# Kernel optimization log

Hardware: AMD Instinct MI355X
Metric: run time of the kernel (lower is better)

Reference implementation:

```python
import jax, jax.numpy as jnp
import numpy as np

N_NODES = 10000
N_EDGES = 100000
D_IN = 2 * 1280   # concat of row/col node embeddings
H1 = 512
H2 = 256


def gcn_conv(x, edge_index, W, b):
    """PyG GCNConv: add self-loops, symmetric deg^-1/2 normalization,
    x @ W then scatter-add of normalized messages, plus bias.
    num_nodes is inferred from x.shape[0] (here = n_edges, faithful to source)."""
    N = x.shape[0]
    loops = jnp.arange(N, dtype=edge_index.dtype)
    row = jnp.concatenate([edge_index[0], loops])  # sources
    col = jnp.concatenate([edge_index[1], loops])  # targets
    deg = jax.ops.segment_sum(jnp.ones_like(row, dtype=x.dtype), col, num_segments=N)
    dinv = jax.lax.rsqrt(deg)  # deg >= 1 thanks to self-loops
    norm = dinv[row] * dinv[col]  # [E+N]
    h = x @ W  # [N, out]
    out = jax.ops.segment_sum(h[row] * norm[:, None], col, num_segments=N)
    return out + b


def setup_inputs() -> dict:
    key = jax.random.key(0)
    ks = jax.random.split(key, 9)
    x = jax.random.normal(ks[0], (N_NODES, 1280), dtype=jnp.float32)
    edge_index = jax.random.randint(ks[1], (2, N_EDGES), 0, N_NODES, dtype=jnp.int32)
    # uniform noise for gumbel-sigmoid (torch.rand); keep strictly in (0,1)
    eps = jax.random.uniform(ks[2], (N_EDGES, 1), jnp.float32, 1e-6, 1.0 - 1e-6)
    W1 = jax.random.normal(ks[3], (D_IN, H1), jnp.float32) * (1.0 / np.sqrt(D_IN))
    b1 = jnp.zeros((H1,), jnp.float32)
    W2 = jax.random.normal(ks[4], (H1, H2), jnp.float32) * (1.0 / np.sqrt(H1))
    b2 = jnp.zeros((H2,), jnp.float32)
    Wl = jax.random.normal(ks[5], (H2, 1), jnp.float32) * (1.0 / np.sqrt(H2))
    bl = jnp.zeros((1,), jnp.float32)
    return {"x": x, "edge_index": edge_index, "eps": eps,
            "W1": W1, "b1": b1, "W2": W2, "b2": b2, "Wl": Wl, "bl": bl}


def reference(x, edge_index, eps, W1, b1, W2, b2, Wl, bl):
    rows, cols = edge_index[0], edge_index[1]
    # per-edge explainer input: concat of endpoint embeddings -> [E, 2560]
    input_embs = jnp.concatenate([x[rows], x[cols]], axis=1)
    h = jax.nn.relu(gcn_conv(input_embs, edge_index, W1, b1))
    h = jax.nn.relu(gcn_conv(h, edge_index, W2, b2))
    pre = h @ Wl + bl  # [E, 1] sampling weights
    # gumbel-sigmoid sampling (temperature = 1.0)
    gate = jnp.log(eps) - jnp.log1p(-eps) + pre
    mask = jax.nn.sigmoid(gate)
    pos, neg = mask, 1.0 - mask
    kld = jnp.mean(pos * jnp.log(pos / 0.5 + 1e-8) + neg * jnp.log(neg / 0.5 + 1e-9))
    return (kld, mask)
```

## Files before the change

kernel.cpp:

```cpp
#include <hip/hip_runtime.h>
#include <cstdint>
#include <cstddef>

#define H1DIM 512
#define H2DIM 256
#define DNODE 1280
#define NPACK 1024

typedef __attribute__((ext_vector_type(8))) short short8v;
typedef __attribute__((ext_vector_type(4))) float f32x4;
typedef __attribute__((ext_vector_type(4))) unsigned short us4;

__device__ __forceinline__ unsigned short f2bf(float f) {
    unsigned int u = __builtin_bit_cast(unsigned int, f);
    u += 0x7fffu + ((u >> 16) & 1u);
    return (unsigned short)(u >> 16);
}
__device__ __forceinline__ float bf2f(unsigned short h) {
    unsigned int u = ((unsigned int)h) << 16;
    return __builtin_bit_cast(float, u);
}

__device__ __forceinline__ int cmi(int R, int kq) {
    return ((R >> 4) << 9) + (((kq >> 3) << 4) + (R & 15)) * 8;
}

__global__ __launch_bounds__(1024) void scan_dinv_k(
    const int* __restrict__ hist, int* __restrict__ off, int* __restrict__ cursor,
    float* __restrict__ dinv, int N)
{
    __shared__ int part[1024];
    const int t = threadIdx.x;
    const int per = (N + 1023) / 1024;
    const int base = t * per;
    int s = 0;
    for (int i = 0; i < per; ++i) { int b = base + i; if (b < N) s += hist[b]; }
    part[t] = s;
    __syncthreads();
    for (int d = 1; d < 1024; d <<= 1) {
        int v = (t >= d) ? part[t - d] : 0;
        __syncthreads();
        part[t] += v;
        __syncthreads();
    }
    int run = (t == 0) ? 0 : part[t - 1];
    for (int i = 0; i < per; ++i) {
        int b = base + i;
        if (b < N) {
            int h = hist[b];
            off[b] = run;
            run += h;
            cursor[b] = 0;
            dinv[b] = rsqrtf(1.0f + (float)h);
        }
    }
    if (t == 1023) off[N] = run;
}
__global__ void fill_k(const int* __restrict__ e0, const int* __restrict__ e1,
                       const int* __restrict__ off, int* __restrict__ cursor,
                       int* __restrict__ srcs, int E) {
    int e = blockIdx.x * 256 + threadIdx.x;
    if (e < E) {
        int t = e1[e];
        int p = off[t] + atomicAdd(&cursor[t], 1);
        srcs[p] = e0[e];
    }
}

__global__ __launch_bounds__(256) void prep_k(
    const float* __restrict__ x, unsigned short* __restrict__ xb, int ncvt, int ntot,
    const int* __restrict__ e1, int* __restrict__ hist, int nhist, int E,
    const float* __restrict__ W1, unsigned short* __restrict__ Bpt1,
    const float* __restrict__ W2, unsigned short* __restrict__ W2t)
{
    __shared__ float tile[32][33];
    int b = blockIdx.x;

    if (b < ncvt) {
        int i = b * 256 + threadIdx.x;
        if (i * 4 < ntot) {
            f32x4 v = *reinterpret_cast<const f32x4*>(x + (size_t)i * 4);
            us4 o;
            o[0] = f2bf(v.x); o[1] = f2bf(v.y); o[2] = f2bf(v.z); o[3] = f2bf(v.w);
            *reinterpret_cast<us4*>(xb + (size_t)i * 4) = o;
        }
        return;
    }
    b -= ncvt;
    if (b < nhist) {
        int e = b * 256 + threadIdx.x;
        if (e < E) atomicAdd(&hist[e1[e]], 1);
        return;
    }
    b -= nhist;

    const float* src; unsigned short* dst; int ldsrc, lddst, bx, by;
    if (b < 640) {
        src = W1; dst = Bpt1; ldsrc = H1DIM; lddst = DNODE; bx = b & 15; by = b >> 4;
    } else if (b < 1280) {
        b -= 640;
        src = W1 + (size_t)DNODE * H1DIM; dst = Bpt1 + (size_t)H1DIM * DNODE;
        ldsrc = H1DIM; lddst = DNODE; bx = b & 15; by = b >> 4;
    } else {
        b -= 1280;
        src = W2; dst = W2t; ldsrc = H2DIM; lddst = H1DIM; bx = b & 7; by = b >> 3;
    }
    const int c0 = bx * 32, r0 = by * 32;
    const int tx = threadIdx.x & 31;
    const int ty = threadIdx.x >> 5;
#pragma unroll
    for (int rr = ty; rr < 32; rr += 8)
        tile[rr][tx] = src[(size_t)(r0 + rr) * ldsrc + c0 + tx];
    __syncthreads();
#pragma unroll
    for (int rr = ty; rr < 32; rr += 8)
        dst[(size_t)(c0 + rr) * lddst + r0 + tx] = f2bf(tile[tx][rr]);
}

template <int MODE>
__global__ __launch_bounds__(512) void gemm_u_k(
    const unsigned short* __restrict__ Ab,
    const unsigned short* __restrict__ Bt,
    unsigned short* __restrict__ Cb,
    const unsigned short* __restrict__ out1b,
    const unsigned short* __restrict__ XWb16,
    const float* __restrict__ b1,
    const float* __restrict__ b2,
    const float* __restrict__ Wl,
    const int* __restrict__ e0, const int* __restrict__ e1,
    unsigned short* __restrict__ h2b, float* __restrict__ pre_raw,
    int M, int K, int Nn, int nwg)
{
    __shared__ alignas(16) unsigned short As[2][128 * 32];
    __shared__ alignas(16) unsigned short Bs[2][256 * 32];
    __shared__ float b1s[H1DIM];
    __shared__ float b2s[H2DIM];
    __shared__ float wls[H2DIM];
    __shared__ float preacc[128];

    const int tid  = threadIdx.x;
    const int lane = tid & 63;
    const int w    = tid >> 6;
    const int wm   = w >> 2, wn = w & 3;

    int mb, n0;
    if (MODE == 0) {
        const int q = nwg >> 3, r = nwg & 7;
        const int xcd = blockIdx.x & 7;
        const int base = (xcd < r) ? xcd * (q + 1) : r * (q + 1) + (xcd - r) * q;
        const int wg = base + (blockIdx.x >> 3);
        mb = wg >> 2;
        n0 = (wg & 3) << 8;
    } else {
        mb = blockIdx.x;
        n0 = 0;
    }
    const int m0 = mb * 128;

    if (MODE == 1) {
        if (tid < 128) preacc[tid] = 0.f;
        if (tid < 256) { b2s[tid] = b2[tid]; wls[tid] = Wl[tid]; }
        b1s[tid] = b1[tid];
    }

    const int sa_r = tid >> 2, sa_k = (tid & 3) << 3;
    const int sb_r = tid >> 1, sb_k = (tid & 1) << 4;
    const int gma  = m0 + sa_r;
    const bool aval = (gma < M);

    const int aw  = cmi(sa_r, sa_k);
    const int bw0 = cmi(sb_r, sb_k);
    const int bw1 = cmi(sb_r, sb_k + 8);

    const unsigned short* bsrc = Bt + (size_t)(n0 + sb_r) * K + sb_k;
    const unsigned short* s1 = nullptr;
    const unsigned short* s2 = nullptr;
    bool dual = false;
    if (MODE == 0) {
        if (aval) s1 = Ab + (size_t)gma * K + sa_k;
    } else if (aval) {
        if (gma < Nn) {
            s1 = out1b + (size_t)gma * H1DIM + sa_k;
        } else {
            s1 = XWb16 + (size_t)e0[gma] * NPACK + sa_k;
            s2 = XWb16 + (size_t)e1[gma] * NPACK + H1DIM + sa_k;
            dual = true;
        }
    }
    if (MODE == 1) __syncthreads();

    f32x4 acc[4][4];
#pragma unroll
    for (int i = 0; i < 4; ++i)
#pragma unroll
        for (int j = 0; j < 4; ++j) acc[i][j] = f32x4{0.f, 0.f, 0.f, 0.f};

    short8v ab1, ab2, bb0, bb1;

    auto load_tile = [&](int k0) {
        bb0 = *reinterpret_cast<const short8v*>(bsrc + k0);
        bb1 = *reinterpret_cast<const short8v*>(bsrc + k0 + 8);
        if (aval) {
            ab1 = *reinterpret_cast<const short8v*>(s1 + k0);
            if (MODE == 1 && dual) ab2 = *reinterpret_cast<const short8v*>(s2 + k0);
        }
    };
    auto write_lds = [&](int buf, int k0) {
        *reinterpret_cast<short8v*>(&Bs[buf][bw0]) = bb0;
        *reinterpret_cast<short8v*>(&Bs[buf][bw1]) = bb1;
        short8v av;
        if (!aval) {
            av = short8v{0,0,0,0,0,0,0,0};
        } else if (MODE == 0 || !dual) {
            av = ab1;
        } else {
#pragma unroll
            for (int ii = 0; ii < 8; ++ii) {
                float v = bf2f((unsigned short)ab1[ii]) + bf2f((unsigned short)ab2[ii])
                        + b1s[k0 + sa_k + ii];
                v = fmaxf(v, 0.f);
                av[ii] = (short)f2bf(v);
            }
        }
        *reinterpret_cast<short8v*>(&As[buf][aw]) = av;
    };

    load_tile(0);
    int buf = 0;
    for (int k0 = 0; k0 < K; k0 += 32) {
        write_lds(buf, k0);
        __syncthreads();
        if (k0 + 32 < K) load_tile(k0 + 32);

        const unsigned short* ard = &As[buf][(wm * 4) * 512 + lane * 8];
        const unsigned short* brd = &Bs[buf][(wn * 4) * 512 + lane * 8];
        short8v af[4], bfq[4];
#pragma unroll
        for (int i = 0; i < 4; ++i)
            af[i] = *reinterpret_cast<const short8v*>(ard + i * 512);
#pragma unroll
        for (int j = 0; j < 4; ++j)
            bfq[j] = *reinterpret_cast<const short8v*>(brd + j * 512);
#pragma unroll
        for (int i = 0; i < 4; ++i)
#pragma unroll
            for (int j = 0; j < 4; ++j)
                acc[i][j] = __builtin_amdgcn_mfma_f32_16x16x32_bf16(af[i], bfq[j], acc[i][j], 0, 0, 0);
        buf ^= 1;
    }

    const int crow0 = m0 + wm * 64 + ((lane >> 4) << 2);
    if (MODE == 0) {
        const int ccol = n0 + wn * 64 + (lane & 15);
#pragma unroll
        for (int i = 0; i < 4; ++i)
#pragma unroll
            for (int q = 0; q < 4; ++q) {
                const int row = crow0 + i * 16 + q;
                if (row < M) {
#pragma unroll
                    for (int j = 0; j < 4; ++j)
                        Cb[(size_t)row * NPACK + ccol + j * 16] = f2bf(acc[i][j][q]);
                }
            }
    } else {
        const int cbase = wn * 64 + (lane & 15);
#pragma unroll
        for (int i = 0; i < 4; ++i)
#pragma unroll
            for (int q = 0; q < 4; ++q) {
                float v = 0.f;
#pragma unroll
                for (int j = 0; j < 4; ++j) {
                    const int c = cbase + j * 16;
                    v += fmaxf(acc[i][j][q] + b2s[c], 0.f) * wls[c];
                }
                v += __shfl_xor(v, 1, 64);
                v += __shfl_xor(v, 2, 64);
                v += __shfl_xor(v, 4, 64);
                v += __shfl_xor(v, 8, 64);
                if ((lane & 15) == 0)
                    atomicAdd(&preacc[wm * 64 + i * 16 + ((lane >> 4) << 2) + q], v);
            }
        if (m0 < Nn) {
            const int ccol = wn * 64 + (lane & 15);
#pragma unroll
            for (int i = 0; i < 4; ++i)
#pragma unroll
                for (int q = 0; q < 4; ++q) {
                    const int row = crow0 + i * 16 + q;
                    if (row < Nn) {
#pragma unroll
                        for (int j = 0; j < 4; ++j)
                            h2b[(size_t)row * H2DIM + ccol + j * 16] = f2bf(acc[i][j][q]);
                    }
                }
        }
        __syncthreads();
        if (tid < 128) {
            const int gm = m0 + tid;
            if (gm >= Nn && gm < M) pre_raw[gm] = preacc[tid];
        }
    }
}

__global__ __launch_bounds__(256) void agg1_k(
    const unsigned short* __restrict__ XWb16, const int* __restrict__ off, const int* __restrict__ srcs,
    const int* __restrict__ e0, const int* __restrict__ e1,
    const float* __restrict__ b1, const float* __restrict__ dinv,
    unsigned short* __restrict__ out1b)
{
    const int t = blockIdx.x;
    const int j = threadIdx.x * 2;
    const int s0 = off[t], s1e = off[t + 1];
    const float dt = dinv[t];
    float ax, ay;
    {
        const unsigned ut = *reinterpret_cast<const unsigned*>(XWb16 + (size_t)e0[t] * NPACK + j);
        const unsigned ub = *reinterpret_cast<const unsigned*>(XWb16 + (size_t)e1[t] * NPACK + H1DIM + j);
        ax = (bf2f((unsigned short)(ut & 0xffff)) + bf2f((unsigned short)(ub & 0xffff))) * dt;
        ay = (bf2f((unsigned short)(ut >> 16))   + bf2f((unsigned short)(ub >> 16)))   * dt;
    }
    for (int i = s0; i < s1e; ++i) {
        const int s = srcs[i];
        const float ds = dinv[s];
        const unsigned ut = *reinterpret_cast<const unsigned*>(XWb16 + (size_t)e0[s] * NPACK + j);
        const unsigned ub = *reinterpret_cast<const unsigned*>(XWb16 + (size_t)e1[s] * NPACK + H1DIM + j);
        ax += (bf2f((unsigned short)(ut & 0xffff)) + bf2f((unsigned short)(ub & 0xffff))) * ds;
        ay += (bf2f((unsigned short)(ut >> 16))   + bf2f((unsigned short)(ub >> 16)))   * ds;
    }
    const float ox = fmaxf(b1[j]     + dt * ax, 0.f);
    const float oy = fmaxf(b1[j + 1] + dt * ay, 0.f);
    const unsigned pk = (unsigned)f2bf(ox) | ((unsigned)f2bf(oy) << 16);
    *reinterpret_cast<unsigned*>(out1b + (size_t)t * H1DIM + j) = pk;
}

__global__ __launch_bounds__(128) void agg2_k(
    const unsigned short* __restrict__ h2b, const int* __restrict__ off, const int* __restrict__ srcs,
    const float* __restrict__ b2, const float* __restrict__ Wl,
    const float* __restrict__ dinv, float* __restrict__ pre_low)
{
    __shared__ float part[2];
    const int t = blockIdx.x;
    const int j = threadIdx.x * 2;
    const int s0 = off[t], s1e = off[t + 1];
    const float dt = dinv[t];
    const unsigned u0 = *reinterpret_cast<const unsigned*>(h2b + (size_t)t * H2DIM + j);
    float ax = bf2f((unsigned short)(u0 & 0xffff)) * dt;
    float ay = bf2f((unsigned short)(u0 >> 16)) * dt;
    for (int i = s0; i < s1e; ++i) {
        const int s = srcs[i];
        const float ds = dinv[s];
        const unsigned v = *reinterpret_cast<const unsigned*>(h2b + (size_t)s * H2DIM + j);
        ax += bf2f((unsigned short)(v & 0xffff)) * ds;
        ay += bf2f((unsigned short)(v >> 16)) * ds;
    }
    float p = fmaxf(b2[j]     + dt * ax, 0.f) * Wl[j]
            + fmaxf(b2[j + 1] + dt * ay, 0.f) * Wl[j + 1];
#pragma unroll
    for (int o = 32; o; o >>= 1) p += __shfl_down(p, o, 64);
    if ((threadIdx.x & 63) == 0) part[threadIdx.x >> 6] = p;
    __syncthreads();
    if (threadIdx.x == 0) pre_low[t] = part[0] + part[1];
}

__global__ __launch_bounds__(256) void final2_k(
    const float* __restrict__ pre_low, const float* __restrict__ pre_raw,
    const float* __restrict__ blp, const float* __restrict__ eps,
    float* __restrict__ dout, int E, int Nn)
{
    __shared__ float part[4];
    const int i = blockIdx.x * 256 + threadIdx.x;
    float kld = 0.f;
    if (i < E) {
        const float pre = ((i < Nn) ? pre_low[i] : pre_raw[i]) + blp[0];
        const float ee = eps[i];
        const float gate = logf(ee) - log1pf(-ee) + pre;
        const float m = 1.0f / (1.0f + expf(-gate));
        dout[1 + i] = m;
        const float pos = m, neg = 1.0f - m;
        kld = pos * logf(pos * 2.0f + 1e-8f) + neg * logf(neg * 2.0f + 1e-9f);
    }
#pragma unroll
    for (int o = 32; o; o >>= 1) kld += __shfl_down(kld, o, 64);
    const int lane = threadIdx.x & 63, wv = threadIdx.x >> 6;
    if (lane == 0) part[wv] = kld;
    __syncthreads();
    if (threadIdx.x == 0)
        atomicAdd(&dout[0], (part[0] + part[1] + part[2] + part[3]) / (float)E);
}

extern "C" void kernel_launch(void* const* d_in, const int* in_sizes, int n_in,
                              void* d_out, int out_size, void* d_ws, size_t ws_size,
                              hipStream_t stream)
{
    const float* x   = (const float*)d_in[0];
    const int*   ei  = (const int*)d_in[1];
    const float* eps = (const float*)d_in[2];
    const float* W1  = (const float*)d_in[3];
    const float* b1  = (const float*)d_in[4];
    const float* W2  = (const float*)d_in[5];
    const float* b2  = (const float*)d_in[6];
    const float* Wl  = (const float*)d_in[7];
    const float* bl  = (const float*)d_in[8];
    float* out = (float*)d_out;
    float* ws  = (float*)d_ws;

    const int N = in_sizes[0] / DNODE;
    const int E = in_sizes[1] / 2;
    const int* e0 = ei;
    const int* e1 = ei + E;

    float* dinv     = ws;
    float* pre_raw  = dinv + 16384;
    float* pre_low  = pre_raw + E;
    float* fend     = pre_low + 16384;
    unsigned short* XWb16 = (unsigned short*)fend;
    unsigned short* out1b = XWb16 + (size_t)N * NPACK;
    unsigned short* h2b   = out1b + (size_t)N * H1DIM;
    unsigned short* xb    = h2b + (size_t)N * H2DIM;
    unsigned short* Bpt1  = xb + (size_t)N * DNODE;
    unsigned short* W2t   = Bpt1 + (size_t)NPACK * DNODE;
    int* hist   = (int*)(W2t + (size_t)H2DIM * H1DIM);
    int* cursor = hist + N;
    int* off    = cursor + N;
    int* srcs   = off + (N + 1);

    hipMemsetAsync(hist, 0, (size_t)N * sizeof(int), stream);
    hipMemsetAsync(out, 0, sizeof(float), stream);

    {
        const int ntot = N * DNODE;
        const int ncvt = (ntot / 4 + 255) / 256;
        const int nhist = (E + 255) / 256;
        const int ntr = 640 + 640 + 128;
        prep_k<<<ncvt + nhist + ntr, 256, 0, stream>>>(
            x, xb, ncvt, ntot, e1, hist, nhist, E, W1, Bpt1, W2, W2t);
    }

    scan_dinv_k<<<1, 1024, 0, stream>>>(hist, off, cursor, dinv, N);
    fill_k<<<(E + 255) / 256, 256, 0, stream>>>(e0, e1, off, cursor, srcs, E);

    {
        const int nwg = 4 * ((N + 127) / 128);
        gemm_u_k<0><<<nwg, 512, 0, stream>>>(
            xb, Bpt1, XWb16, nullptr, nullptr, b1, b2, Wl, e0, e1,
            nullptr, nullptr, N, DNODE, 0, nwg);
    }

    agg1_k<<<N, 256, 0, stream>>>(XWb16, off, srcs, e0, e1, b1, dinv, out1b);

    {
        const int nwg = (E + 127) / 128;
        gemm_u_k<1><<<nwg, 512, 0, stream>>>(
            nullptr, W2t, nullptr, out1b, XWb16, b1, b2, Wl, e0, e1,
            h2b, pre_raw, E, H1DIM, N, nwg);
    }

    agg2_k<<<N, 128, 0, stream>>>(h2b, off, srcs, b2, Wl, dinv, pre_low);

    final2_k<<<(E + 255) / 256, 256, 0, stream>>>(pre_low, pre_raw, bl, eps, out, E, N);
}
```

Baseline: 217.3 us.

## Fold scan into GEMM launch, precompute scaled H1 rows, merge fill into builder

The degree scan/dinv kernel becomes an extra workgroup of the first GEMM launch, and the CSR fill kernel is merged into a new kernel that also builds a per-node pre-scaled H1 row (sum of top and bottom XW halves times dinv). The first aggregation then gathers one contiguous 512-wide bf16 row per neighbour instead of two indirect half-rows plus a dinv lookup. This removes two launches and halves the gather traffic in agg1. The cost is an extra N×512 bf16 buffer write and read, plus one extra rounding to bf16 before accumulation.

```diff
diff --git a/kernel.cpp b/kernel.cpp
--- a/kernel.cpp
+++ b/kernel.cpp
@@ -23,48 +23,6 @@
 
 __device__ __forceinline__ int cmi(int R, int kq) {
     return ((R >> 4) << 9) + (((kq >> 3) << 4) + (R & 15)) * 8;
-}
-
-__global__ __launch_bounds__(1024) void scan_dinv_k(
-    const int* __restrict__ hist, int* __restrict__ off, int* __restrict__ cursor,
-    float* __restrict__ dinv, int N)
-{
-    __shared__ int part[1024];
-    const int t = threadIdx.x;
-    const int per = (N + 1023) / 1024;
-    const int base = t * per;
-    int s = 0;
-    for (int i = 0; i < per; ++i) { int b = base + i; if (b < N) s += hist[b]; }
-    part[t] = s;
-    __syncthreads();
-    for (int d = 1; d < 1024; d <<= 1) {
-        int v = (t >= d) ? part[t - d] : 0;
-        __syncthreads();
-        part[t] += v;
-        __syncthreads();
-    }
-    int run = (t == 0) ? 0 : part[t - 1];
-    for (int i = 0; i < per; ++i) {
-        int b = base + i;
-        if (b < N) {
-            int h = hist[b];
-            off[b] = run;
-            run += h;
-            cursor[b] = 0;
-            dinv[b] = rsqrtf(1.0f + (float)h);
-        }
-    }
-    if (t == 1023) off[N] = run;
-}
-__global__ void fill_k(const int* __restrict__ e0, const int* __restrict__ e1,
-                       const int* __restrict__ off, int* __restrict__ cursor,
-                       int* __restrict__ srcs, int E) {
-    int e = blockIdx.x * 256 + threadIdx.x;
-    if (e < E) {
-        int t = e1[e];
-        int p = off[t] + atomicAdd(&cursor[t], 1);
-        srcs[p] = e0[e];
-    }
 }
 
 __global__ __launch_bounds__(256) void prep_k(
@@ -129,8 +87,42 @@
     const float* __restrict__ Wl,
     const int* __restrict__ e0, const int* __restrict__ e1,
     unsigned short* __restrict__ h2b, float* __restrict__ pre_raw,
+    int* __restrict__ hist, int* __restrict__ off, int* __restrict__ cursor,
+    float* __restrict__ dinv,
     int M, int K, int Nn, int nwg)
 {
+    const int tid  = threadIdx.x;
+
+    if (MODE == 0 && blockIdx.x >= nwg) {
+        __shared__ int part[512];
+        const int t = tid;
+        const int per = (Nn + 511) / 512;
+        const int base = t * per;
+        int s = 0;
+        for (int i = 0; i < per; ++i) { int b = base + i; if (b < Nn) s += hist[b]; }
+        part[t] = s;
+        __syncthreads();
+        for (int d = 1; d < 512; d <<= 1) {
+            int v = (t >= d) ? part[t - d] : 0;
+            __syncthreads();
+            part[t] += v;
+            __syncthreads();
+        }
+        int run = (t == 0) ? 0 : part[t - 1];
+        for (int i = 0; i < per; ++i) {
+            int b = base + i;
+            if (b < Nn) {
+                int h = hist[b];
+                off[b] = run;
+                run += h;
+                cursor[b] = 0;
+                dinv[b] = rsqrtf(1.0f + (float)h);
+            }
+        }
+        if (t == 511) off[Nn] = run;
+        return;
+    }
+
     __shared__ alignas(16) unsigned short As[2][128 * 32];
     __shared__ alignas(16) unsigned short Bs[2][256 * 32];
     __shared__ float b1s[H1DIM];
@@ -138,7 +130,6 @@
     __shared__ float wls[H2DIM];
     __shared__ float preacc[128];
 
-    const int tid  = threadIdx.x;
     const int lane = tid & 63;
     const int w    = tid >> 6;
     const int wm   = w >> 2, wn = w & 3;
@@ -304,9 +295,38 @@
     }
 }
 
+__global__ __launch_bounds__(256) void build1_fill_k(
+    const unsigned short* __restrict__ XWb16, const float* __restrict__ dinv,
+    const int* __restrict__ e0, const int* __restrict__ e1,
+    unsigned short* __restrict__ H1b,
+    const int* __restrict__ off, int* __restrict__ cursor, int* __restrict__ srcs,
+    int N, int E)
+{
+    int b = blockIdx.x;
+    if (b < N) {
+        const int a = e0[b], c = e1[b];
+        const float dv = dinv[b];
+        const unsigned short* pt = XWb16 + (size_t)a * NPACK;
+        const unsigned short* pb = XWb16 + (size_t)c * NPACK + H1DIM;
+        const int j = threadIdx.x * 2;
+        const unsigned ut = *reinterpret_cast<const unsigned*>(pt + j);
+        const unsigned ub = *reinterpret_cast<const unsigned*>(pb + j);
+        const float ox = (bf2f((unsigned short)(ut & 0xffff)) + bf2f((unsigned short)(ub & 0xffff))) * dv;
+        const float oy = (bf2f((unsigned short)(ut >> 16))   + bf2f((unsigned short)(ub >> 16)))   * dv;
+        const unsigned pk = (unsigned)f2bf(ox) | ((unsigned)f2bf(oy) << 16);
+        *reinterpret_cast<unsigned*>(H1b + (size_t)b * H1DIM + j) = pk;
+        return;
+    }
+    int e = (b - N) * 256 + threadIdx.x;
+    if (e < E) {
+        int t = e1[e];
+        int p = off[t] + atomicAdd(&cursor[t], 1);
+        srcs[p] = e0[e];
+    }
+}
+
 __global__ __launch_bounds__(256) void agg1_k(
-    const unsigned short* __restrict__ XWb16, const int* __restrict__ off, const int* __restrict__ srcs,
-    const int* __restrict__ e0, const int* __restrict__ e1,
+    const unsigned short* __restrict__ H1b, const int* __restrict__ off, const int* __restrict__ srcs,
     const float* __restrict__ b1, const float* __restrict__ dinv,
     unsigned short* __restrict__ out1b)
 {
@@ -314,20 +334,13 @@
     const int j = threadIdx.x * 2;
     const int s0 = off[t], s1e = off[t + 1];
     const float dt = dinv[t];
-    float ax, ay;
-    {
-        const unsigned ut = *reinterpret_cast<const unsigned*>(XWb16 + (size_t)e0[t] * NPACK + j);
-        const unsigned ub = *reinterpret_cast<const unsigned*>(XWb16 + (size_t)e1[t] * NPACK + H1DIM + j);
-        ax = (bf2f((unsigned short)(ut & 0xffff)) + bf2f((unsigned short)(ub & 0xffff))) * dt;
-        ay = (bf2f((unsigned short)(ut >> 16))   + bf2f((unsigned short)(ub >> 16)))   * dt;
-    }
+    const unsigned u0 = *reinterpret_cast<const unsigned*>(H1b + (size_t)t * H1DIM + j);
+    float ax = bf2f((unsigned short)(u0 & 0xffff));
+    float ay = bf2f((unsigned short)(u0 >> 16));
     for (int i = s0; i < s1e; ++i) {
-        const int s = srcs[i];
-        const float ds = dinv[s];
-        const unsigned ut = *reinterpret_cast<const unsigned*>(XWb16 + (size_t)e0[s] * NPACK + j);
-        const unsigned ub = *reinterpret_cast<const unsigned*>(XWb16 + (size_t)e1[s] * NPACK + H1DIM + j);
-        ax += (bf2f((unsigned short)(ut & 0xffff)) + bf2f((unsigned short)(ub & 0xffff))) * ds;
-        ay += (bf2f((unsigned short)(ut >> 16))   + bf2f((unsigned short)(ub >> 16)))   * ds;
+        const unsigned v = *reinterpret_cast<const unsigned*>(H1b + (size_t)srcs[i] * H1DIM + j);
+        ax += bf2f((unsigned short)(v & 0xffff));
+        ay += bf2f((unsigned short)(v >> 16));
     }
     const float ox = fmaxf(b1[j]     + dt * ax, 0.f);
     const float oy = fmaxf(b1[j + 1] + dt * ay, 0.f);
@@ -417,7 +430,8 @@
     float* fend     = pre_low + 16384;
     unsigned short* XWb16 = (unsigned short*)fend;
     unsigned short* out1b = XWb16 + (size_t)N * NPACK;
-    unsigned short* h2b   = out1b + (size_t)N * H1DIM;
+    unsigned short* H1b   = out1b + (size_t)N * H1DIM;
+    unsigned short* h2b   = H1b + (size_t)N * H1DIM;
     unsigned short* xb    = h2b + (size_t)N * H2DIM;
     unsigned short* Bpt1  = xb + (size_t)N * DNODE;
     unsigned short* W2t   = Bpt1 + (size_t)NPACK * DNODE;
@@ -438,23 +452,23 @@
             x, xb, ncvt, ntot, e1, hist, nhist, E, W1, Bpt1, W2, W2t);
     }
 
-    scan_dinv_k<<<1, 1024, 0, stream>>>(hist, off, cursor, dinv, N);
-    fill_k<<<(E + 255) / 256, 256, 0, stream>>>(e0, e1, off, cursor, srcs, E);
-
     {
         const int nwg = 4 * ((N + 127) / 128);
-        gemm_u_k<0><<<nwg, 512, 0, stream>>>(
+        gemm_u_k<0><<<nwg + 1, 512, 0, stream>>>(
             xb, Bpt1, XWb16, nullptr, nullptr, b1, b2, Wl, e0, e1,
-            nullptr, nullptr, N, DNODE, 0, nwg);
-    }
-
-    agg1_k<<<N, 256, 0, stream>>>(XWb16, off, srcs, e0, e1, b1, dinv, out1b);
+            nullptr, nullptr, hist, off, cursor, dinv, N, DNODE, N, nwg);
+    }
+
+    build1_fill_k<<<N + (E + 255) / 256, 256, 0, stream>>>(
+        XWb16, dinv, e0, e1, H1b, off, cursor, srcs, N, E);
+
+    agg1_k<<<N, 256, 0, stream>>>(H1b, off, srcs, b1, dinv, out1b);
 
     {
         const int nwg = (E + 127) / 128;
         gemm_u_k<1><<<nwg, 512, 0, stream>>>(
             nullptr, W2t, nullptr, out1b, XWb16, b1, b2, Wl, e0, e1,
-            h2b, pre_raw, E, H1DIM, N, nwg);
+            h2b, pre_raw, nullptr, nullptr, nullptr, nullptr, E, H1DIM, N, nwg);
     }
 
     agg2_k<<<N, 128, 0, stream>>>(h2b, off, srcs, b2, Wl, dinv, pre_low);
```

After: 193.2 us. 11.1% less time.
